# Optimization experiments

Hardware: AMD Instinct MI355X
Metric: run time of the kernel (lower is better)

Reference implementation:

```python
import jax, jax.numpy as jnp
import numpy as np
import math

H = 8  # n_heads

def rel_shift(x):
    # x: [B, H, U, P] -> Transformer-XL relative shift
    B, h, U, P = x.shape
    x = jnp.pad(x, ((0, 0), (0, 0), (0, 0), (1, 0)))  # zero-pad front of last dim
    x = x.reshape(B, h, P + 1, U)[:, :, 1:, :].reshape(B, h, U, P)
    return x

def setup_inputs() -> dict:
    key = jax.random.key(0)
    ks = jax.random.split(key, 16)
    B, T, D = 8, 1024, 512
    s = 0.05  # weight scale ~ xavier for D=512
    inp = {
        'q': jax.random.normal(ks[0], (B, T, D), jnp.float32),
        'k': jax.random.normal(ks[1], (B, T, D), jnp.float32),
        'v': jax.random.normal(ks[2], (B, T, D), jnp.float32),
        'pos': jax.random.normal(ks[3], (T, D), jnp.float32),
        'mask': jax.random.randint(ks[4], (B, T, T), 0, 2).astype(jnp.int32),
        'Wq': jax.random.normal(ks[5], (D, D), jnp.float32) * s,
        'bq': jnp.zeros((D,), jnp.float32),
        'Wk': jax.random.normal(ks[6], (D, D), jnp.float32) * s,
        'bk': jnp.zeros((D,), jnp.float32),
        'Wv': jax.random.normal(ks[7], (D, D), jnp.float32) * s,
        'bv': jnp.zeros((D,), jnp.float32),
        'Wo': jax.random.normal(ks[8], (D, D), jnp.float32) * s,
        'bo': jnp.zeros((D,), jnp.float32),
        'Wp': jax.random.normal(ks[9], (D, D), jnp.float32) * s,
        'bias_u': jax.random.normal(ks[10], (H, D // H), jnp.float32) * s,
        'bias_v': jax.random.normal(ks[11], (H, D // H), jnp.float32) * s,
    }
    return inp

def reference(q, k, v, pos, mask, Wq, bq, Wk, bk, Wv, bv, Wo, bo, Wp, bias_u, bias_v):
    B, T, D = q.shape
    dk = D // H
    qh = (q @ Wq.T + bq).reshape(B, T, H, dk)   # B U H d
    kh = (k @ Wk.T + bk).reshape(B, T, H, dk)   # B T H d
    vh = (v @ Wv.T + bv).reshape(B, T, H, dk)   # B T H d
    ph = (pos @ Wp.T).reshape(T, H, dk)          # P H d (shared across batch)
    q_u = qh + bias_u                            # B U H d
    q_v = qh + bias_v
    ac = jnp.einsum('buhd,bthd->bhut', q_u, kh)  # content term
    bd = jnp.einsum('buhd,phd->bhup', q_v, ph)   # position term
    bd = rel_shift(bd)[:, :, :, :T]
    scores = (ac + bd) / math.sqrt(dk)           # B H U T
    m = (mask[:, None, :, :] == 0)               # B 1 U T
    neg = jnp.finfo(scores.dtype).min
    scores = jnp.where(m, neg, scores)
    attn = jax.nn.softmax(scores, axis=-1)
    attn = jnp.where(m, 0.0, attn)
    x = jnp.einsum('bhut,bthd->buhd', attn, vh).reshape(B, T, D)
    return x @ Wo.T + bo
```

## Files before the change

### kernel.cpp

```cpp
#include <hip/hip_runtime.h>
#include <stdint.h>

#define Bc 8
#define Tc 1024
#define Dc 512
#define Hc 8

typedef __bf16 bf16x8 __attribute__((ext_vector_type(8)));
typedef float f32x4 __attribute__((ext_vector_type(4)));
typedef unsigned short ushort8v __attribute__((ext_vector_type(8)));

#define NEGBF 0xF14Au

__device__ __forceinline__ unsigned short f2bf(float f) {
    union { float f; uint32_t u; } v; v.f = f;
    uint32_t u = v.u;
    u += 0x7fffu + ((u >> 16) & 1u);
    return (unsigned short)(u >> 16);
}
__device__ __forceinline__ unsigned short f2bf_native(float f) {
    __bf16 b = (__bf16)f;
    return *(unsigned short*)&b;
}
__device__ __forceinline__ f32x4 mfma16(bf16x8 a, bf16x8 b, f32x4 c) {
    return __builtin_amdgcn_mfma_f32_16x16x32_bf16(a, b, c, 0, 0, 0);
}
__device__ __forceinline__ void gl16(const unsigned short* g, unsigned short* l) {
    __builtin_amdgcn_global_load_lds(
        (const __attribute__((address_space(1))) uint32_t*)g,
        (__attribute__((address_space(3))) uint32_t*)l, 16, 0, 0);
}

#define SC2 0.1803368801f

__global__ __launch_bounds__(256) void prep(
    const int* __restrict__ mask, uint32_t* __restrict__ bits,
    const float* __restrict__ Wq, const float* __restrict__ Wk,
    const float* __restrict__ Wv, const float* __restrict__ Wp,
    const float* __restrict__ Wo, unsigned short* __restrict__ Wb,
    const float* __restrict__ q, const float* __restrict__ k,
    const float* __restrict__ v, const float* __restrict__ p,
    unsigned short* __restrict__ qb, unsigned short* __restrict__ kb,
    unsigned short* __restrict__ vb, unsigned short* __restrict__ pb)
{
    int bid = blockIdx.x;
    if (bid < 32768) {
        int wid = (bid * 256 + threadIdx.x) >> 6;
        int lane = threadIdx.x & 63;
        unsigned long long bl = __ballot(mask[(size_t)wid * 64 + lane] != 0);
        if (lane == 0)  bits[wid * 2]     = (uint32_t)bl;
        if (lane == 32) bits[wid * 2 + 1] = (uint32_t)(bl >> 32);
    } else if (bid < 33408) {
        int i = (bid - 32768) * 2048 + threadIdx.x * 8;
        int m = i >> 18, r = i & 262143;
        const float* Ws[5] = {Wq, Wk, Wv, Wp, Wo};
        const float* s = Ws[m] + r;
        ushort8v o;
#pragma unroll
        for (int j = 0; j < 8; ++j) o[j] = f2bf(s[j]);
        *(ushort8v*)(Wb + i) = o;
    } else {
        size_t i = (size_t)(bid - 33408) * 2048 + threadIdx.x * 8;
        const float* src; unsigned short* dst; size_t off;
        if (i < 4194304)       { src = q; dst = qb; off = i; }
        else if (i < 8388608)  { src = k; dst = kb; off = i - 4194304; }
        else if (i < 12582912) { src = v; dst = vb; off = i - 8388608; }
        else                   { src = p; dst = pb; off = i - 12582912; }
        ushort8v o;
#pragma unroll
        for (int j = 0; j < 8; ++j) o[j] = f2bf(src[off + j]);
        *(ushort8v*)(dst + off) = o;
    }
}

__global__ __launch_bounds__(256) void proj4(
    const unsigned short* __restrict__ qb, const unsigned short* __restrict__ kb,
    const unsigned short* __restrict__ vb, const unsigned short* __restrict__ pb,
    const unsigned short* __restrict__ Wb,
    const float* __restrict__ bq, const float* __restrict__ bk,
    const float* __restrict__ bv,
    const float* __restrict__ bias_u, const float* __restrict__ bias_v,
    unsigned short* __restrict__ qu, unsigned short* __restrict__ qv,
    unsigned short* __restrict__ kh, unsigned short* __restrict__ vT,
    unsigned short* __restrict__ ph)
{
    int id = blockIdx.x;
    int wg = (id & 7) * 200 + (id >> 3);
    int z, rem;
    if (wg < 512)       { z = 0; rem = wg; }
    else if (wg < 1024) { z = 1; rem = wg - 512; }
    else if (wg < 1536) { z = 2; rem = wg - 1024; }
    else                { z = 3; rem = wg - 1536; }
    const int m0 = (rem & 3) * 128, n0 = (rem >> 2) * 64;
    const unsigned short* A = z == 0 ? qb : z == 1 ? kb : z == 2 ? vb : pb;
    const unsigned short* W = Wb + (size_t)z * 262144;

    __shared__ unsigned short As[2][64][64];
    __shared__ unsigned short Bs[2][128][64];
    const int tid = threadIdx.x, lane = tid & 63, wave = tid >> 6;
    const int lrow = lane & 15, lkg = lane >> 4;
    const int wr = (wave >> 1) * 32, wc = (wave & 1) * 64;
    const int srow = lane >> 3;
    const int scol = ((lane & 7) ^ (srow & 7)) * 8;
    const int swr  = (lrow & 7) * 8;

    f32x4 acc[2][4];
#pragma unroll
    for (int i = 0; i < 2; ++i)
#pragma unroll
        for (int j = 0; j < 4; ++j) acc[i][j] = f32x4{0.f, 0.f, 0.f, 0.f};

#pragma unroll
    for (int it = 0; it < 2; ++it) {
        int r8 = (wave * 2 + it) * 8;
        gl16(A + (size_t)(n0 + r8 + srow) * 512 + scol, &As[0][r8][0]);
    }
#pragma unroll
    for (int it = 0; it < 4; ++it) {
        int r8 = (wave * 4 + it) * 8;
        gl16(W + (size_t)(m0 + r8 + srow) * 512 + scol, &Bs[0][r8][0]);
    }

    int cur = 0;
    for (int kt = 0; kt < 512; kt += 64) {
        if (kt + 64 < 512) {
#pragma unroll
            for (int it = 0; it < 2; ++it) {
                int r8 = (wave * 2 + it) * 8;
                gl16(A + (size_t)(n0 + r8 + srow) * 512 + kt + 64 + scol, &As[cur ^ 1][r8][0]);
            }
#pragma unroll
            for (int it = 0; it < 4; ++it) {
                int r8 = (wave * 4 + it) * 8;
                gl16(W + (size_t)(m0 + r8 + srow) * 512 + kt + 64 + scol, &Bs[cur ^ 1][r8][0]);
            }
            asm volatile("s_waitcnt vmcnt(6)" ::: "memory");
        } else {
            asm volatile("s_waitcnt vmcnt(0)" ::: "memory");
        }
        __builtin_amdgcn_s_barrier();
#pragma unroll
        for (int kk = 0; kk < 2; ++kk) {
            bf16x8 a[2], bb[4];
#pragma unroll
            for (int i = 0; i < 2; ++i)
                a[i] = *(const bf16x8*)&As[cur][wr + i * 16 + lrow][(kk * 32 + lkg * 8) ^ swr];
#pragma unroll
            for (int j = 0; j < 4; ++j)
                bb[j] = *(const bf16x8*)&Bs[cur][wc + j * 16 + lrow][(kk * 32 + lkg * 8) ^ swr];
#pragma unroll
            for (int i = 0; i < 2; ++i)
#pragma unroll
                for (int j = 0; j < 4; ++j)
                    acc[i][j] = mfma16(a[i], bb[j], acc[i][j]);
        }
        asm volatile("s_waitcnt lgkmcnt(0)" ::: "memory");
        __builtin_amdgcn_s_barrier();
        cur ^= 1;
    }

#pragma unroll
    for (int i = 0; i < 2; ++i) {
        int nbase = n0 + wr + i * 16 + lkg * 4;
#pragma unroll
        for (int j = 0; j < 4; ++j) {
            int m = m0 + wc + j * 16 + lrow;
            float bb = z == 0 ? bq[m] : z == 1 ? bk[m] : z == 2 ? bv[m] : 0.f;
            float bu = 0.f, bvv = 0.f;
            if (z == 0) { bu = bias_u[m]; bvv = bias_v[m]; }
#pragma unroll
            for (int qq = 0; qq < 4; ++qq) {
                int n = nbase + qq;
                float c = acc[i][j][qq] + bb;
                if (z == 0) {
                    qu[(size_t)n * 512 + m] = f2bf(c + bu);
                    qv[(size_t)n * 512 + m] = f2bf(c + bvv);
                } else if (z == 1) {
                    kh[(size_t)n * 512 + m] = f2bf(c * SC2);
                } else if (z == 2) {
                    int b = n >> 10, t = n & 1023, h = m >> 6, d = m & 63;
                    vT[(((size_t)((b * 8 + h) * 64 + d)) << 10) + t] = f2bf(c);
                } else {
                    ph[(size_t)n * 512 + m] = f2bf(c);
                }
            }
        }
    }
}

__global__ __launch_bounds__(256) void gemm_out(
    const unsigned short* __restrict__ X, const unsigned short* __restrict__ Wob,
    const float* __restrict__ bo, float* __restrict__ fout)
{
    int id = blockIdx.x;
    int wg = (id & 7) * 64 + (id >> 3);
    const int m0 = (wg & 3) * 128, n0 = (wg >> 2) * 64;
    __shared__ unsigned short As[2][64][64];
    __shared__ unsigned short Bs[2][128][64];
    const int tid = threadIdx.x, lane = tid & 63, wave = tid >> 6;
    const int lrow = lane & 15, lkg = lane >> 4;
    const int wr = (wave >> 1) * 32, wc = (wave & 1) * 64;
    const int srow = lane >> 3;
    const int scol = ((lane & 7) ^ (srow & 7)) * 8;
    const int swr  = (lrow & 7) * 8;

    f32x4 acc[2][4];
#pragma unroll
    for (int i = 0; i < 2; ++i)
#pragma unroll
        for (int j = 0; j < 4; ++j) acc[i][j] = f32x4{0.f, 0.f, 0.f, 0.f};

#pragma unroll
    for (int it = 0; it < 2; ++it) {
        int r8 = (wave * 2 + it) * 8;
        gl16(X + (size_t)(n0 + r8 + srow) * 512 + scol, &As[0][r8][0]);
    }
#pragma unroll
    for (int it = 0; it < 4; ++it) {
        int r8 = (wave * 4 + it) * 8;
        gl16(Wob + (size_t)(m0 + r8 + srow) * 512 + scol, &Bs[0][r8][0]);
    }

    int cur = 0;
    for (int kt = 0; kt < 512; kt += 64) {
        if (kt + 64 < 512) {
#pragma unroll
            for (int it = 0; it < 2; ++it) {
                int r8 = (wave * 2 + it) * 8;
                gl16(X + (size_t)(n0 + r8 + srow) * 512 + kt + 64 + scol, &As[cur ^ 1][r8][0]);
            }
#pragma unroll
            for (int it = 0; it < 4; ++it) {
                int r8 = (wave * 4 + it) * 8;
                gl16(Wob + (size_t)(m0 + r8 + srow) * 512 + kt + 64 + scol, &Bs[cur ^ 1][r8][0]);
            }
            asm volatile("s_waitcnt vmcnt(6)" ::: "memory");
        } else {
            asm volatile("s_waitcnt vmcnt(0)" ::: "memory");
        }
        __builtin_amdgcn_s_barrier();
#pragma unroll
        for (int kk = 0; kk < 2; ++kk) {
            bf16x8 a[2], bb[4];
#pragma unroll
            for (int i = 0; i < 2; ++i)
                a[i] = *(const bf16x8*)&As[cur][wr + i * 16 + lrow][(kk * 32 + lkg * 8) ^ swr];
#pragma unroll
            for (int j = 0; j < 4; ++j)
                bb[j] = *(const bf16x8*)&Bs[cur][wc + j * 16 + lrow][(kk * 32 + lkg * 8) ^ swr];
#pragma unroll
            for (int i = 0; i < 2; ++i)
#pragma unroll
                for (int j = 0; j < 4; ++j)
                    acc[i][j] = mfma16(a[i], bb[j], acc[i][j]);
        }
        asm volatile("s_waitcnt lgkmcnt(0)" ::: "memory");
        __builtin_amdgcn_s_barrier();
        cur ^= 1;
    }
#pragma unroll
    for (int i = 0; i < 2; ++i) {
        int nbase = n0 + wr + i * 16 + lkg * 4;
#pragma unroll
        for (int j = 0; j < 4; ++j) {
            int m = m0 + wc + j * 16 + lrow;
            float bb = bo[m];
#pragma unroll
            for (int qq = 0; qq < 4; ++qq)
                fout[(size_t)(nbase + qq) * 512 + m] = acc[i][j][qq] + bb;
        }
    }
}

__global__ __launch_bounds__(256) void bd_gemm(
    const unsigned short* __restrict__ qv, const unsigned short* __restrict__ ph,
    const uint32_t* __restrict__ mbits, unsigned short* __restrict__ bds,
    int bh_base)
{
    int id = blockIdx.x, wg;
    if (gridDim.x == 4096) wg = (id & 7) * 512 + (id >> 3);
    else                   wg = (id & 7) * 64 + (id >> 3);
    const int zz = wg >> 6, rem = wg & 63;
    const int u0 = (rem & 7) * 128, p0 = (rem >> 3) * 128;
    const int bh = bh_base + zz;
    const int b = bh >> 3, h = bh & 7;
    __shared__ unsigned short As[128][64];
    __shared__ unsigned short Bs[128][64];
    const int tid = threadIdx.x, lane = tid & 63, wave = tid >> 6;
    const int lrow = lane & 15, lkg = lane >> 4;
    const int wr = (wave >> 1) * 64, wc = (wave & 1) * 64;
    const int srow = lane >> 3, scol = (lane & 7) * 8;

#pragma unroll
    for (int it = 0; it < 4; ++it) {
        int r8 = (wave * 4 + it) * 8;
        gl16(qv + ((size_t)(b * 1024 + u0 + r8 + srow)) * 512 + h * 64 + scol, &As[r8][0]);
        gl16(ph + ((size_t)(p0 + r8 + srow)) * 512 + h * 64 + scol, &Bs[r8][0]);
    }
    __syncthreads();

    f32x4 acc[4][4];
#pragma unroll
    for (int i = 0; i < 4; ++i)
#pragma unroll
        for (int j = 0; j < 4; ++j) acc[i][j] = f32x4{0.f, 0.f, 0.f, 0.f};
#pragma unroll
    for (int kk = 0; kk < 2; ++kk) {
        bf16x8 a[4], bb[4];
#pragma unroll
        for (int i = 0; i < 4; ++i)
            a[i] = *(const bf16x8*)&As[wr + i * 16 + lrow][kk * 32 + lkg * 8];
#pragma unroll
        for (int j = 0; j < 4; ++j)
            bb[j] = *(const bf16x8*)&Bs[wc + j * 16 + lrow][kk * 32 + lkg * 8];
#pragma unroll
        for (int i = 0; i < 4; ++i)
#pragma unroll
            for (int j = 0; j < 4; ++j)
                acc[i][j] = mfma16(a[i], bb[j], acc[i][j]);
    }

    unsigned short* slab = bds + ((size_t)zz << 20);
    const uint32_t* mb = mbits + ((size_t)b << 15);
    const int Cbase = 1025 * (u0 + wr + lkg * 4) + (p0 + wc + lrow) - 1023;
#pragma unroll
    for (int i = 0; i < 4; ++i) {
#pragma unroll
        for (int qq = 0; qq < 4; ++qq) {
            int Fb = Cbase + 1025 * (i * 16 + qq);
            int w0 = Fb >> 5;
            uint32_t mw0 = mb[w0], mw1 = mb[w0 + 1], mw2 = mb[w0 + 2];
            uint64_t m01 = ((uint64_t)mw1 << 32) | mw0;
            uint64_t m12 = ((uint64_t)mw2 << 32) | mw1;
            int sh = Fb & 31;
#pragma unroll
            for (int j = 0; j < 4; ++j) {
                uint32_t bit = (j < 2) ? ((uint32_t)(m01 >> (sh + j * 16)) & 1u)
                                       : ((uint32_t)(m12 >> (sh + (j - 2) * 16)) & 1u);
                unsigned short val = bit ? f2bf_native(acc[i][j][qq] * SC2)
                                         : (unsigned short)NEGBF;
                int F = Fb + j * 16;
                if (F >= 0) slab[F] = val;
            }
        }
    }

    if (p0 == 0 && tid < 128) {
        int ud = u0 + tid;
        if (ud < 1023) {
            const uint8_t* mrowbytes = (const uint8_t*)mbits + ((size_t)b << 17);
            uint32_t bit = (mrowbytes[ud * 128 + ((ud + 1) >> 3)] >> ((ud + 1) & 7)) & 1;
            slab[((size_t)ud << 10) + (ud + 1)] = bit ? 0 : (unsigned short)NEGBF;
        }
    }
}

__global__ __launch_bounds__(256, 4) void attn10(
    const unsigned short* __restrict__ qu, const unsigned short* __restrict__ kh,
    const unsigned short* __restrict__ vT, const unsigned short* __restrict__ bds,
    unsigned short* __restrict__ xout, int b_base)
{
    int id = blockIdx.x, nid, b, rem;
    if (gridDim.x == 1024) {
        nid = (id & 7) * 128 + (id >> 3);
        b = b_base + (nid >> 7); rem = nid & 127;
    } else {
        nid = (id & 7) * 16 + (id >> 3);
        b = b_base; rem = nid;
    }
    const int h = rem >> 4, ublk = rem & 15;
    const int u0 = ublk * 64;

    __shared__ unsigned short Ks[2][64][64];
    __shared__ unsigned short Vs[2][64][64];
    __shared__ unsigned short Ps[4][16][64];
    const int tid = threadIdx.x, lane = tid & 63, wave = tid >> 6;
    const int lrow = lane & 15, lkg = lane >> 4;
    const int srow = lane >> 3;
    const int scol = ((lane & 7) ^ (srow & 7)) * 8;
    const int swr  = (lrow & 7) * 8;
    const f32x4 zero = {0.f, 0.f, 0.f, 0.f};

    const unsigned short* qub = qu + ((size_t)(b * 1024 + u0 + wave * 16 + lrow)) * 512 + h * 64;
    bf16x8 au0 = *(const bf16x8*)(qub + lkg * 8);
    bf16x8 au1 = *(const bf16x8*)(qub + 32 + lkg * 8);

    const int urow = u0 + wave * 16 + lkg * 4;
    const int zoff = (b - b_base) * 8 + h;
    const unsigned short* bdp[4];
#pragma unroll
    for (int q = 0; q < 4; ++q)
        bdp[q] = bds + ((size_t)zoff << 20) + (((size_t)(urow + q)) << 10) + lrow;
    const unsigned short* kbase = kh + ((size_t)(b * 1024)) * 512 + h * 64;
    const unsigned short* vbase = vT + (((size_t)((b * 8 + h) * 64)) << 10);

    f32x4 acc[4] = {zero, zero, zero, zero};
    float lsum[4] = {0.f, 0.f, 0.f, 0.f};

#pragma unroll
    for (int it = 0; it < 2; ++it) {
        int r8 = (wave * 2 + it) * 8;
        gl16(kbase + (size_t)(r8 + srow) * 512 + scol, &Ks[0][r8][0]);
        gl16(vbase + ((size_t)(r8 + srow) << 10) + scol, &Vs[0][r8][0]);
    }

    int cur = 0;
    for (int t0 = 0; t0 < 1024; t0 += 64) {
        f32x4 bdC[4];
#pragma unroll
        for (int j = 0; j < 4; ++j)
#pragma unroll
            for (int q = 0; q < 4; ++q)
                bdC[j][q] = __uint_as_float(((uint32_t)bdp[q][j * 16]) << 16);
#pragma unroll
        for (int q = 0; q < 4; ++q) bdp[q] += 64;

        if (t0 < 960) {
#pragma unroll
            for (int it = 0; it < 2; ++it) {
                int r8 = (wave * 2 + it) * 8;
                gl16(kbase + (size_t)(t0 + 64 + r8 + srow) * 512 + scol, &Ks[cur ^ 1][r8][0]);
                gl16(vbase + ((size_t)(r8 + srow) << 10) + t0 + 64 + scol, &Vs[cur ^ 1][r8][0]);
            }
            asm volatile("s_waitcnt vmcnt(4)" ::: "memory");
        } else {
            asm volatile("s_waitcnt vmcnt(0)" ::: "memory");
        }
        __builtin_amdgcn_s_barrier();

        f32x4 s[4];
#pragma unroll
        for (int j = 0; j < 4; ++j) {
            bf16x8 k0 = *(const bf16x8*)&Ks[cur][j * 16 + lrow][(lkg * 8) ^ swr];
            bf16x8 k1 = *(const bf16x8*)&Ks[cur][j * 16 + lrow][(32 + lkg * 8) ^ swr];
            s[j] = mfma16(au1, k1, mfma16(au0, k0, bdC[j]));
        }
#pragma unroll
        for (int j = 0; j < 4; ++j) {
#pragma unroll
            for (int q = 0; q < 4; ++q) {
                float p = exp2f(s[j][q]);
                lsum[q] += p;
                int prow = lkg * 4 + q;
                Ps[wave][prow][(j * 16 + lrow) ^ ((prow & 7) * 8)] = f2bf_native(p);
            }
        }
        bf16x8 pa0 = *(const bf16x8*)&Ps[wave][lrow][(lkg * 8) ^ swr];
        bf16x8 pa1 = *(const bf16x8*)&Ps[wave][lrow][(32 + lkg * 8) ^ swr];
#pragma unroll
        for (int jj = 0; jj < 4; ++jj) {
            bf16x8 vb0 = *(const bf16x8*)&Vs[cur][jj * 16 + lrow][(lkg * 8) ^ swr];
            bf16x8 vb1 = *(const bf16x8*)&Vs[cur][jj * 16 + lrow][(32 + lkg * 8) ^ swr];
            acc[jj] = mfma16(pa1, vb1, mfma16(pa0, vb0, acc[jj]));
        }
        asm volatile("s_waitcnt lgkmcnt(0)" ::: "memory");
        __builtin_amdgcn_s_barrier();
        cur ^= 1;
    }

#pragma unroll
    for (int off = 1; off < 16; off <<= 1)
#pragma unroll
        for (int q = 0; q < 4; ++q) lsum[q] += __shfl_xor(lsum[q], off);
#pragma unroll
    for (int q = 0; q < 4; ++q) {
        float inv = 1.0f / lsum[q];
        int u = urow + q;
#pragma unroll
        for (int jj = 0; jj < 4; ++jj) {
            int d = jj * 16 + lrow;
            xout[((size_t)(b * 1024 + u)) * 512 + h * 64 + d] = f2bf_native(acc[jj][q] * inv);
        }
    }
}

extern "C" void kernel_launch(void* const* d_in, const int* in_sizes, int n_in,
                              void* d_out, int out_size, void* d_ws, size_t ws_size,
                              hipStream_t stream) {
    const float* q    = (const float*)d_in[0];
    const float* k    = (const float*)d_in[1];
    const float* v    = (const float*)d_in[2];
    const float* pos  = (const float*)d_in[3];
    const int*   mask = (const int*)d_in[4];
    const float* Wq   = (const float*)d_in[5];
    const float* bq   = (const float*)d_in[6];
    const float* Wk   = (const float*)d_in[7];
    const float* bk   = (const float*)d_in[8];
    const float* Wv   = (const float*)d_in[9];
    const float* bv   = (const float*)d_in[10];
    const float* Wo   = (const float*)d_in[11];
    const float* bo   = (const float*)d_in[12];
    const float* Wp   = (const float*)d_in[13];
    const float* bias_u = (const float*)d_in[14];
    const float* bias_v = (const float*)d_in[15];
    float* out = (float*)d_out;

    unsigned short* ws = (unsigned short*)d_ws;
    constexpr size_t NQ  = (size_t)Bc * Tc * Dc;
    constexpr size_t NP  = (size_t)Tc * Dc;
    constexpr size_t NMB = (size_t)Bc * Tc * 32;
    constexpr size_t NWB = (size_t)5 * 262144;
    unsigned short* ws_qu = ws;
    unsigned short* ws_qv = ws_qu + NQ;
    unsigned short* ws_kh = ws_qv + NQ;
    unsigned short* ws_vT = ws_kh + NQ;
    unsigned short* ws_ph = ws_vT + NQ;
    uint32_t*       ws_mb = (uint32_t*)(ws_ph + NP);
    unsigned short* ws_wb = (unsigned short*)(ws_mb + NMB);
    unsigned short* ws_qb = ws_wb + NWB;
    unsigned short* ws_kb = ws_qb + NQ;
    unsigned short* ws_vb = ws_kb + NQ;
    unsigned short* ws_pb = ws_vb + NQ;
    unsigned short* ws_bd = ws_qb;

    constexpr size_t BD_FULL  = (size_t)64 * 1024 * 1024;
    constexpr size_t BD_SMALL = (size_t)8 * 1024 * 1024;
    const size_t base_bytes = (4 * NQ + NP + NWB) * 2 + NMB * 4;
    const bool full  = ws_size >= base_bytes + BD_FULL * 2;
    const bool tier2 = !full && ws_size >= base_bytes + ((3 * NQ + NP) + NQ) * 2;

    dim3 blk(256);
    prep<<<39808, blk, 0, stream>>>(mask, ws_mb, Wq, Wk, Wv, Wp, Wo, ws_wb,
                                    q, k, v, pos, ws_qb, ws_kb, ws_vb, ws_pb);
    proj4<<<1600, blk, 0, stream>>>(ws_qb, ws_kb, ws_vb, ws_pb, ws_wb, bq, bk, bv,
                                    bias_u, bias_v, ws_qu, ws_qv, ws_kh, ws_vT, ws_ph);

    if (full) {
        unsigned short* ws_x = ws_qv;
        bd_gemm<<<4096, blk, 0, stream>>>(ws_qv, ws_ph, ws_mb, ws_bd, 0);
        attn10<<<1024, blk, 0, stream>>>(ws_qu, ws_kh, ws_vT, ws_bd, ws_x, 0);
        gemm_out<<<512, blk, 0, stream>>>(ws_x, ws_wb + 4 * 262144, bo, out);
    } else if (tier2) {
        unsigned short* ws_x = ws_qb + 3 * NQ + NP;
        for (int b = 0; b < 8; ++b) {
            bd_gemm<<<512, blk, 0, stream>>>(ws_qv, ws_ph, ws_mb, ws_bd, b * 8);
            attn10<<<128, blk, 0, stream>>>(ws_qu, ws_kh, ws_vT, ws_bd, ws_x, b);
        }
        gemm_out<<<512, blk, 0, stream>>>(ws_x, ws_wb + 4 * 262144, bo, out);
    }
}
```

Baseline: 174.2 us.

## Retile bd_gemm to 16-row strips with double-buffered swizzled pos tiles

```diff
diff --git a/kernel.cpp b/kernel.cpp
--- a/kernel.cpp
+++ b/kernel.cpp
@@ -280,73 +280,85 @@
     int id = blockIdx.x, wg;
     if (gridDim.x == 4096) wg = (id & 7) * 512 + (id >> 3);
     else                   wg = (id & 7) * 64 + (id >> 3);
-    const int zz = wg >> 6, rem = wg & 63;
-    const int u0 = (rem & 7) * 128, p0 = (rem >> 3) * 128;
+    const int zz = wg >> 6, ut = wg & 63;
+    const int u_base = ut * 16;
     const int bh = bh_base + zz;
     const int b = bh >> 3, h = bh & 7;
-    __shared__ unsigned short As[128][64];
-    __shared__ unsigned short Bs[128][64];
+    __shared__ unsigned short Bs[2][128][64];
     const int tid = threadIdx.x, lane = tid & 63, wave = tid >> 6;
     const int lrow = lane & 15, lkg = lane >> 4;
-    const int wr = (wave >> 1) * 64, wc = (wave & 1) * 64;
-    const int srow = lane >> 3, scol = (lane & 7) * 8;
+    const int srow = lane >> 3;
+    const int scol = ((lane & 7) ^ (srow & 7)) * 8;
+    const int swr  = (lrow & 7) * 8;
+
+    const unsigned short* qvb = qv + ((size_t)(b * 1024 + u_base + lrow)) * 512 + h * 64;
+    bf16x8 a0 = *(const bf16x8*)(qvb + lkg * 8);
+    bf16x8 a1 = *(const bf16x8*)(qvb + 32 + lkg * 8);
+
+    f32x4 acc[16];
+#pragma unroll
+    for (int jj = 0; jj < 16; ++jj) acc[jj] = f32x4{0.f, 0.f, 0.f, 0.f};
 
 #pragma unroll
     for (int it = 0; it < 4; ++it) {
-        int r8 = (wave * 4 + it) * 8;
-        gl16(qv + ((size_t)(b * 1024 + u0 + r8 + srow)) * 512 + h * 64 + scol, &As[r8][0]);
-        gl16(ph + ((size_t)(p0 + r8 + srow)) * 512 + h * 64 + scol, &Bs[r8][0]);
-    }
-    __syncthreads();
-
-    f32x4 acc[4][4];
-#pragma unroll
-    for (int i = 0; i < 4; ++i)
-#pragma unroll
-        for (int j = 0; j < 4; ++j) acc[i][j] = f32x4{0.f, 0.f, 0.f, 0.f};
-#pragma unroll
-    for (int kk = 0; kk < 2; ++kk) {
-        bf16x8 a[4], bb[4];
-#pragma unroll
-        for (int i = 0; i < 4; ++i)
-            a[i] = *(const bf16x8*)&As[wr + i * 16 + lrow][kk * 32 + lkg * 8];
-#pragma unroll
-        for (int j = 0; j < 4; ++j)
-            bb[j] = *(const bf16x8*)&Bs[wc + j * 16 + lrow][kk * 32 + lkg * 8];
-#pragma unroll
-        for (int i = 0; i < 4; ++i)
-#pragma unroll
-            for (int j = 0; j < 4; ++j)
-                acc[i][j] = mfma16(a[i], bb[j], acc[i][j]);
+        int r8 = wave * 32 + it * 8;
+        gl16(ph + ((size_t)(r8 + srow)) * 512 + h * 64 + scol, &Bs[0][r8][0]);
+    }
+
+#pragma unroll
+    for (int c = 0; c < 8; ++c) {
+        if (c < 7) {
+#pragma unroll
+            for (int it = 0; it < 4; ++it) {
+                int r8 = wave * 32 + it * 8;
+                gl16(ph + ((size_t)((c + 1) * 128 + r8 + srow)) * 512 + h * 64 + scol,
+                     &Bs[(c + 1) & 1][r8][0]);
+            }
+            asm volatile("s_waitcnt vmcnt(4)" ::: "memory");
+        } else {
+            asm volatile("s_waitcnt vmcnt(0)" ::: "memory");
+        }
+        __builtin_amdgcn_s_barrier();
+#pragma unroll
+        for (int kk = 0; kk < 2; ++kk) {
+            bf16x8 av = kk ? a1 : a0;
+#pragma unroll
+            for (int jt = 0; jt < 2; ++jt) {
+                bf16x8 bb = *(const bf16x8*)
+                    &Bs[c & 1][wave * 32 + jt * 16 + lrow][(kk * 32 + lkg * 8) ^ swr];
+                acc[c * 2 + jt] = mfma16(av, bb, acc[c * 2 + jt]);
+            }
+        }
+        asm volatile("s_waitcnt lgkmcnt(0)" ::: "memory");
+        __builtin_amdgcn_s_barrier();
     }
 
     unsigned short* slab = bds + ((size_t)zz << 20);
     const uint32_t* mb = mbits + ((size_t)b << 15);
-    const int Cbase = 1025 * (u0 + wr + lkg * 4) + (p0 + wc + lrow) - 1023;
-#pragma unroll
-    for (int i = 0; i < 4; ++i) {
-#pragma unroll
-        for (int qq = 0; qq < 4; ++qq) {
-            int Fb = Cbase + 1025 * (i * 16 + qq);
+    const int Fq0 = 1025 * (u_base + lkg * 4) + wave * 32 + lrow - 1023;
+#pragma unroll
+    for (int q = 0; q < 4; ++q) {
+        int Fq = Fq0 + 1025 * q;
+#pragma unroll
+        for (int c = 0; c < 8; ++c) {
+            int Fb = Fq + c * 128;
             int w0 = Fb >> 5;
-            uint32_t mw0 = mb[w0], mw1 = mb[w0 + 1], mw2 = mb[w0 + 2];
+            uint32_t mw0 = mb[w0], mw1 = mb[w0 + 1];
             uint64_t m01 = ((uint64_t)mw1 << 32) | mw0;
-            uint64_t m12 = ((uint64_t)mw2 << 32) | mw1;
             int sh = Fb & 31;
 #pragma unroll
-            for (int j = 0; j < 4; ++j) {
-                uint32_t bit = (j < 2) ? ((uint32_t)(m01 >> (sh + j * 16)) & 1u)
-                                       : ((uint32_t)(m12 >> (sh + (j - 2) * 16)) & 1u);
-                unsigned short val = bit ? f2bf_native(acc[i][j][qq] * SC2)
+            for (int hhf = 0; hhf < 2; ++hhf) {
+                uint32_t bit = (uint32_t)(m01 >> (sh + hhf * 16)) & 1u;
+                unsigned short val = bit ? f2bf_native(acc[c * 2 + hhf][q] * SC2)
                                          : (unsigned short)NEGBF;
-                int F = Fb + j * 16;
+                int F = Fb + hhf * 16;
                 if (F >= 0) slab[F] = val;
             }
         }
     }
 
-    if (p0 == 0 && tid < 128) {
-        int ud = u0 + tid;
+    if (tid < 16) {
+        int ud = u_base + tid;
         if (ud < 1023) {
             const uint8_t* mrowbytes = (const uint8_t*)mbits + ((size_t)b << 17);
             uint32_t bit = (mrowbytes[ud * 128 + ((ud + 1) >> 3)] >> ((ud + 1) & 7)) & 1;
```

After: 195.5 us. 1.12x slower.
